# Kernel tuning notes

Measured on AMD Instinct MI355X. Metric: run time of the kernel, lower is better.

The kernel has to match this reference:

```python
import jax, jax.numpy as jnp
import numpy as np

IN_FEATURES = 4096
OUT_FEATURES = 2048
N_GROUPS = 16  # group size = IN_FEATURES // N_GROUPS = 256


def setup_inputs() -> dict:
    key = jax.random.key(0)
    k1, k2, k3, k4 = jax.random.split(key, 4)
    x = jax.random.normal(k1, (8, 64, IN_FEATURES), dtype=jnp.float32)
    # uint8 quantized weights, stored [out, in] as in the torch module
    qweight = jax.random.randint(k2, (OUT_FEATURES, IN_FEATURES), 0, 256).astype(jnp.uint8)
    # per-(out-channel, group) dequant scale and offset; scale ~ (max-min)/255 of rand weights
    qrange = jax.random.uniform(k3, (OUT_FEATURES, N_GROUPS), dtype=jnp.float32) * (2.0 / 255.0)
    qmin = -jax.random.uniform(k4, (OUT_FEATURES, N_GROUPS), dtype=jnp.float32)
    return {"x": x, "qweight": qweight, "qrange": qrange, "qmin": qmin}


def reference(x, qweight, qrange, qmin):
    # out[b,s,o] = sum_i x[b,s,i] * (q[o,i]*qrange[o,g(i)] + qmin[o,g(i)])
    B, S, IN = x.shape
    OUT, G = qrange.shape
    gs = IN // G
    xg = x.reshape(B, S, G, gs)                     # [B,S,G,gs]
    qg = qweight.reshape(OUT, G, gs).astype(x.dtype)  # [O,G,gs]
    # fused per-group dequant matmul: scale folded into the contraction
    out = jnp.einsum('bsgi,ogi,og->bso', xg, qg, qrange)
    # offset term: qmin[o,g] * sum_i_in_group x[b,s,i]
    out = out + jnp.einsum('bsg,og->bso', xg.sum(axis=-1), qmin)
    return out
```

## Files before the change

kernel.cpp:

```cpp
#include <hip/hip_runtime.h>
#include <hip/hip_bf16.h>


#define M_T 512
#define N_T 2048
#define K_T 4096
#define NGRP 16
#define BM 128
#define BN 128
#define BK 64
#define OUT_ELEMS (M_T * N_T)
#define W_ELEMS (N_T * K_T)
#define X_ELEMS (M_T * K_T)

typedef __attribute__((ext_vector_type(8))) short mfrag_t;
typedef __attribute__((ext_vector_type(8))) unsigned short u16x8;
typedef __attribute__((ext_vector_type(4))) float f32x4;

__device__ __forceinline__ unsigned short f2bf(float f) {
  union { __hip_bfloat16 h; unsigned short u; } c;
  c.h = __float2bfloat16(f);
  return c.u;
}

__device__ __forceinline__ float bf2f(unsigned short u) {
  union { unsigned int i; float f; } c;
  c.i = ((unsigned int)u) << 16;
  return c.f;
}

__global__ __launch_bounds__(256) void pack_kernel(
    const float* __restrict__ x, const int* __restrict__ qw,
    const float* __restrict__ qrange, const float* __restrict__ qmin,
    unsigned short* __restrict__ wsW, unsigned short* __restrict__ wsX) {
  const int bid = blockIdx.x;
  const int tid = threadIdx.x;
  if (bid < (W_ELEMS / 8) / 256) {
    const int gidx = bid * 256 + tid;
    const int o = gidx >> 9;
    const int k8 = gidx & 511;
    const int g = k8 >> 5;
    const float sc = qrange[o * NGRP + g];
    const float mn = qmin[o * NGRP + g];
    const int4* q = (const int4*)(qw + ((size_t)o << 12) + (k8 << 3));
    const int4 q0 = q[0], q1 = q[1];
    u16x8 p;
    p[0] = f2bf((float)q0.x * sc + mn); p[1] = f2bf((float)q0.y * sc + mn);
    p[2] = f2bf((float)q0.z * sc + mn); p[3] = f2bf((float)q0.w * sc + mn);
    p[4] = f2bf((float)q1.x * sc + mn); p[5] = f2bf((float)q1.y * sc + mn);
    p[6] = f2bf((float)q1.z * sc + mn); p[7] = f2bf((float)q1.w * sc + mn);
    *(u16x8*)(wsW + ((size_t)gidx << 3)) = p;
  } else {
    const int gidx = (bid - (W_ELEMS / 8) / 256) * 256 + tid;
    const float4* a = (const float4*)(x + ((size_t)gidx << 3));
    const float4 a0 = a[0], a1 = a[1];
    u16x8 p;
    p[0] = f2bf(a0.x); p[1] = f2bf(a0.y); p[2] = f2bf(a0.z); p[3] = f2bf(a0.w);
    p[4] = f2bf(a1.x); p[5] = f2bf(a1.y); p[6] = f2bf(a1.z); p[7] = f2bf(a1.w);
    *(u16x8*)(wsX + ((size_t)gidx << 3)) = p;
  }
}

template <int KSPLIT, bool XCDSWZ>
__global__ __launch_bounds__(512, 4) void dq_gemm_kernel(
    const unsigned short* __restrict__ wsX, const unsigned short* __restrict__ wsW,
    unsigned short* __restrict__ dst) {
  constexpr int KC = K_T / KSPLIT;
  constexpr int NTC = KC / BK;

  __shared__ __align__(16) unsigned short As[BM * BK];
  __shared__ __align__(16) unsigned short Bs[BN * BK];

  const int tid = threadIdx.x;
  int xt, yt, kc;
  if (XCDSWZ) {
    const int b = blockIdx.x;
    kc = b & 7;
    const int slot = b >> 3;
    xt = slot & 15;
    yt = slot >> 4;
  } else {
    const int b = blockIdx.x;
    xt = b & 15;
    yt = (b >> 4) & 3;
    kc = b >> 6;
  }
  const int n0 = xt * BN;
  const int m0 = yt * BM;
  const int kbase = kc * KC;

  const int lane = tid & 63;
  const int wv = tid >> 6;
  const int wm = (wv >> 2) * 64;
  const int wn = (wv & 3) * 32;
  const int lr = lane & 15;
  const int lq = lane >> 4;
  const int rxl = lr & 7;

  const int swzcol = (((lane & 7) ^ (lane >> 3)) << 3);
  const int r0 = wv * 16 + (lane >> 3);
  const int r1 = r0 + 8;
  const unsigned short* gA0 = wsX + (size_t)(m0 + r0) * K_T + kbase + swzcol;
  const unsigned short* gA1 = wsX + (size_t)(m0 + r1) * K_T + kbase + swzcol;
  const unsigned short* gB0 = wsW + (size_t)(n0 + r0) * K_T + kbase + swzcol;
  const unsigned short* gB1 = wsW + (size_t)(n0 + r1) * K_T + kbase + swzcol;
  unsigned short* lA0 = &As[wv * 1024];
  unsigned short* lA1 = &As[wv * 1024 + 512];
  unsigned short* lB0 = &Bs[wv * 1024];
  unsigned short* lB1 = &Bs[wv * 1024 + 512];

#define STAGE(T)                                                              \
  do {                                                                        \
    const size_t o_ = (size_t)(T) * BK;                                       \
    __builtin_amdgcn_global_load_lds(                                         \
        (const __attribute__((address_space(1))) void*)(gA0 + o_),            \
        (__attribute__((address_space(3))) void*)lA0, 16, 0, 0);              \
    __builtin_amdgcn_global_load_lds(                                         \
        (const __attribute__((address_space(1))) void*)(gA1 + o_),            \
        (__attribute__((address_space(3))) void*)lA1, 16, 0, 0);              \
    __builtin_amdgcn_global_load_lds(                                         \
        (const __attribute__((address_space(1))) void*)(gB0 + o_),            \
        (__attribute__((address_space(3))) void*)lB0, 16, 0, 0);              \
    __builtin_amdgcn_global_load_lds(                                         \
        (const __attribute__((address_space(1))) void*)(gB1 + o_),            \
        (__attribute__((address_space(3))) void*)lB1, 16, 0, 0);              \
  } while (0)

  f32x4 acc[4][2] = {};

  STAGE(0);
  for (int t = 0; t < NTC; ++t) {
    __syncthreads();

#pragma unroll
    for (int kk = 0; kk < 2; ++kk) {
      const int so = ((kk * 4 + lq) ^ rxl) << 3;
      mfrag_t af[4], bf[2];
#pragma unroll
      for (int fm = 0; fm < 4; ++fm)
        af[fm] = *(const mfrag_t*)&As[(wm + fm * 16 + lr) * BK + so];
#pragma unroll
      for (int fn = 0; fn < 2; ++fn)
        bf[fn] = *(const mfrag_t*)&Bs[(wn + fn * 16 + lr) * BK + so];
#pragma unroll
      for (int fm = 0; fm < 4; ++fm)
#pragma unroll
        for (int fn = 0; fn < 2; ++fn)
          acc[fm][fn] = __builtin_amdgcn_mfma_f32_16x16x32_bf16(af[fm], bf[fn], acc[fm][fn], 0, 0, 0);
    }

    if (t + 1 < NTC) {
      __syncthreads();
      STAGE(t + 1);
    }
  }
#undef STAGE

  unsigned short* base = dst + (size_t)kc * OUT_ELEMS;
#pragma unroll
  for (int fm = 0; fm < 4; ++fm) {
#pragma unroll
    for (int fn = 0; fn < 2; ++fn) {
      const int rr = m0 + wm + fm * 16 + lq * 4;
      const int c = n0 + wn + fn * 16 + lr;
      unsigned short* op = base + (size_t)rr * N_T + c;
      op[0 * (size_t)N_T] = f2bf(acc[fm][fn][0]);
      op[1 * (size_t)N_T] = f2bf(acc[fm][fn][1]);
      op[2 * (size_t)N_T] = f2bf(acc[fm][fn][2]);
      op[3 * (size_t)N_T] = f2bf(acc[fm][fn][3]);
    }
  }
}

template <int KSPLIT>
__global__ __launch_bounds__(256) void reduce_kernel(const unsigned short* __restrict__ ws,
                                                     float* __restrict__ out) {
  const int i8 = blockIdx.x * 256 + threadIdx.x;
  const size_t base = (size_t)i8 * 8;
  float s[8];
  {
    const u16x8 v = *(const u16x8*)(ws + base);
#pragma unroll
    for (int j = 0; j < 8; ++j) s[j] = bf2f(v[j]);
  }
#pragma unroll
  for (int sl = 1; sl < KSPLIT; ++sl) {
    const u16x8 v = *(const u16x8*)(ws + (size_t)sl * OUT_ELEMS + base);
#pragma unroll
    for (int j = 0; j < 8; ++j) s[j] += bf2f(v[j]);
  }
  float4* o = (float4*)(out + base);
  o[0] = make_float4(s[0], s[1], s[2], s[3]);
  o[1] = make_float4(s[4], s[5], s[6], s[7]);
}

__global__ void naive_kernel(const float* __restrict__ x, const int* __restrict__ qw,
                             const float* __restrict__ qrange, const float* __restrict__ qmin,
                             float* __restrict__ out) {
  const int idx = blockIdx.x * 256 + threadIdx.x;
  if (idx >= OUT_ELEMS) return;
  const int m = idx / N_T, n = idx % N_T;
  float s = 0.f;
  for (int g = 0; g < NGRP; ++g) {
    const float sc = qrange[n * NGRP + g], mn = qmin[n * NGRP + g];
    float d = 0.f, xs = 0.f;
    for (int k = g * 256; k < (g + 1) * 256; ++k) {
      d += x[(size_t)m * K_T + k] * (float)qw[(size_t)n * K_T + k];
      xs += x[(size_t)m * K_T + k];
    }
    s += d * sc + xs * mn;
  }
  out[idx] = s;
}

extern "C" void kernel_launch(void* const* d_in, const int* in_sizes, int n_in,
                              void* d_out, int out_size, void* d_ws, size_t ws_size,
                              hipStream_t stream) {
  const float* x = (const float*)d_in[0];
  const int* qw = (const int*)d_in[1];
  const float* qr = (const float*)d_in[2];
  const float* qm = (const float*)d_in[3];
  float* out = (float*)d_out;

  constexpr int KS = 8;
  unsigned short* wsW = (unsigned short*)d_ws;
  unsigned short* wsX = wsW + W_ELEMS;
  unsigned short* partials = wsX + X_ELEMS;
  const size_t need = (size_t)W_ELEMS * 2 + (size_t)X_ELEMS * 2 +
                      (size_t)KS * OUT_ELEMS * 2;
  if (ws_size >= need) {
    const int packblk = (W_ELEMS / 8) / 256 + (X_ELEMS / 8) / 256;
    pack_kernel<<<packblk, 256, 0, stream>>>(x, qw, qr, qm, wsW, wsX);
    const int nblk = (N_T / BN) * (M_T / BM) * KS;
    dq_gemm_kernel<KS, true><<<nblk, dim3(512, 1, 1), 0, stream>>>(wsX, wsW, partials);
    reduce_kernel<KS><<<OUT_ELEMS / 8 / 256, 256, 0, stream>>>(partials, out);
  } else {
    naive_kernel<<<(OUT_ELEMS + 255) / 256, 256, 0, stream>>>(x, qw, qr, qm, out);
  }
}
```

Measured before the change: 32.27 us.

## Enlarge GEMM M-tile to 256 with 64x64 per-wave tiles

Doubles the block tile in M from 128 to 256 and reorganizes the 8 waves into a 4x2 grid of 64x64 sub-tiles, so each wave computes 16 MFMA accumulators instead of 8. Global-to-LDS staging is restructured to match, and launch bounds are relaxed to 2 blocks per CU. The goal is more reuse of each LDS fragment per MFMA and less load traffic per unit of output. In exchange, register pressure and LDS use per block go up, and the grid halves to 256 blocks, which cuts parallelism across CUs.

```diff
diff --git a/kernel.cpp b/kernel.cpp
--- a/kernel.cpp
+++ b/kernel.cpp
@@ -6,7 +6,7 @@
 #define N_T 2048
 #define K_T 4096
 #define NGRP 16
-#define BM 128
+#define BM 256
 #define BN 128
 #define BK 64
 #define OUT_ELEMS (M_T * N_T)
@@ -61,8 +61,8 @@
   }
 }
 
-template <int KSPLIT, bool XCDSWZ>
-__global__ __launch_bounds__(512, 4) void dq_gemm_kernel(
+template <int KSPLIT>
+__global__ __launch_bounds__(512, 2) void dq_gemm_kernel(
     const unsigned short* __restrict__ wsX, const unsigned short* __restrict__ wsW,
     unsigned short* __restrict__ dst) {
   constexpr int KC = K_T / KSPLIT;
@@ -72,61 +72,47 @@
   __shared__ __align__(16) unsigned short Bs[BN * BK];
 
   const int tid = threadIdx.x;
-  int xt, yt, kc;
-  if (XCDSWZ) {
-    const int b = blockIdx.x;
-    kc = b & 7;
-    const int slot = b >> 3;
-    xt = slot & 15;
-    yt = slot >> 4;
-  } else {
-    const int b = blockIdx.x;
-    xt = b & 15;
-    yt = (b >> 4) & 3;
-    kc = b >> 6;
-  }
+  const int b = blockIdx.x;
+  const int kc = b & 7;
+  const int slot = b >> 3;
+  const int xt = slot & 15;
+  const int yt = slot >> 4;
   const int n0 = xt * BN;
   const int m0 = yt * BM;
   const int kbase = kc * KC;
 
   const int lane = tid & 63;
   const int wv = tid >> 6;
-  const int wm = (wv >> 2) * 64;
-  const int wn = (wv & 3) * 32;
+
+  const int wm = (wv >> 1) * 64;
+  const int wn = (wv & 1) * 64;
   const int lr = lane & 15;
   const int lq = lane >> 4;
   const int rxl = lr & 7;
 
-  const int swzcol = (((lane & 7) ^ (lane >> 3)) << 3);
-  const int r0 = wv * 16 + (lane >> 3);
-  const int r1 = r0 + 8;
-  const unsigned short* gA0 = wsX + (size_t)(m0 + r0) * K_T + kbase + swzcol;
-  const unsigned short* gA1 = wsX + (size_t)(m0 + r1) * K_T + kbase + swzcol;
-  const unsigned short* gB0 = wsW + (size_t)(n0 + r0) * K_T + kbase + swzcol;
-  const unsigned short* gB1 = wsW + (size_t)(n0 + r1) * K_T + kbase + swzcol;
-  unsigned short* lA0 = &As[wv * 1024];
-  unsigned short* lA1 = &As[wv * 1024 + 512];
-  unsigned short* lB0 = &Bs[wv * 1024];
-  unsigned short* lB1 = &Bs[wv * 1024 + 512];
+  const int srow8 = lane >> 3;
+  const int scol = (((lane & 7) ^ srow8) << 3);
+  const unsigned short* gA = wsX + (size_t)(m0 + wv * 32 + srow8) * K_T + kbase + scol;
+  const unsigned short* gB = wsW + (size_t)(n0 + wv * 16 + srow8) * K_T + kbase + scol;
+  unsigned short* lA = &As[wv * 32 * BK];
+  unsigned short* lB = &Bs[wv * 16 * BK];
 
 #define STAGE(T)                                                              \
   do {                                                                        \
     const size_t o_ = (size_t)(T) * BK;                                       \
-    __builtin_amdgcn_global_load_lds(                                         \
-        (const __attribute__((address_space(1))) void*)(gA0 + o_),            \
-        (__attribute__((address_space(3))) void*)lA0, 16, 0, 0);              \
-    __builtin_amdgcn_global_load_lds(                                         \
-        (const __attribute__((address_space(1))) void*)(gA1 + o_),            \
-        (__attribute__((address_space(3))) void*)lA1, 16, 0, 0);              \
-    __builtin_amdgcn_global_load_lds(                                         \
-        (const __attribute__((address_space(1))) void*)(gB0 + o_),            \
-        (__attribute__((address_space(3))) void*)lB0, 16, 0, 0);              \
-    __builtin_amdgcn_global_load_lds(                                         \
-        (const __attribute__((address_space(1))) void*)(gB1 + o_),            \
-        (__attribute__((address_space(3))) void*)lB1, 16, 0, 0);              \
+    _Pragma("unroll")                                                         \
+    for (int c_ = 0; c_ < 4; ++c_)                                            \
+      __builtin_amdgcn_global_load_lds(                                       \
+          (const __attribute__((address_space(1))) void*)(gA + o_ + (size_t)c_ * 8 * K_T), \
+          (__attribute__((address_space(3))) void*)(lA + c_ * 8 * BK), 16, 0, 0); \
+    _Pragma("unroll")                                                         \
+    for (int c_ = 0; c_ < 2; ++c_)                                            \
+      __builtin_amdgcn_global_load_lds(                                       \
+          (const __attribute__((address_space(1))) void*)(gB + o_ + (size_t)c_ * 8 * K_T), \
+          (__attribute__((address_space(3))) void*)(lB + c_ * 8 * BK), 16, 0, 0); \
   } while (0)
 
-  f32x4 acc[4][2] = {};
+  f32x4 acc[4][4] = {};
 
   STAGE(0);
   for (int t = 0; t < NTC; ++t) {
@@ -135,17 +121,17 @@
 #pragma unroll
     for (int kk = 0; kk < 2; ++kk) {
       const int so = ((kk * 4 + lq) ^ rxl) << 3;
-      mfrag_t af[4], bf[2];
+      mfrag_t af[4], bf[4];
 #pragma unroll
       for (int fm = 0; fm < 4; ++fm)
         af[fm] = *(const mfrag_t*)&As[(wm + fm * 16 + lr) * BK + so];
 #pragma unroll
-      for (int fn = 0; fn < 2; ++fn)
+      for (int fn = 0; fn < 4; ++fn)
         bf[fn] = *(const mfrag_t*)&Bs[(wn + fn * 16 + lr) * BK + so];
 #pragma unroll
       for (int fm = 0; fm < 4; ++fm)
 #pragma unroll
-        for (int fn = 0; fn < 2; ++fn)
+        for (int fn = 0; fn < 4; ++fn)
           acc[fm][fn] = __builtin_amdgcn_mfma_f32_16x16x32_bf16(af[fm], bf[fn], acc[fm][fn], 0, 0, 0);
     }
 
@@ -160,7 +146,7 @@
 #pragma unroll
   for (int fm = 0; fm < 4; ++fm) {
 #pragma unroll
-    for (int fn = 0; fn < 2; ++fn) {
+    for (int fn = 0; fn < 4; ++fn) {
       const int rr = m0 + wm + fm * 16 + lq * 4;
       const int c = n0 + wn + fn * 16 + lr;
       unsigned short* op = base + (size_t)rr * N_T + c;
@@ -232,7 +218,7 @@
     const int packblk = (W_ELEMS / 8) / 256 + (X_ELEMS / 8) / 256;
     pack_kernel<<<packblk, 256, 0, stream>>>(x, qw, qr, qm, wsW, wsX);
     const int nblk = (N_T / BN) * (M_T / BM) * KS;
-    dq_gemm_kernel<KS, true><<<nblk, dim3(512, 1, 1), 0, stream>>>(wsX, wsW, partials);
+    dq_gemm_kernel<KS><<<nblk, dim3(512, 1, 1), 0, stream>>>(wsX, wsW, partials);
     reduce_kernel<KS><<<OUT_ELEMS / 8 / 256, 256, 0, stream>>>(partials, out);
   } else {
     naive_kernel<<<(OUT_ELEMS + 255) / 256, 256, 0, stream>>>(x, qw, qr, qm, out);
```

After: 34.58 us. +7.2%, slower.

## Fuse weight dequantization into GEMM main loop, pack weights as uint8

Applied to the files above, without the earlier changes.

The pack kernel no longer dequantizes the weights to bf16. It only narrows the int32 quantized weights to a uint8 workspace. The GEMM kernel now loads the uint8 weight tile through registers, applies the per-group scale and offset, and writes bf16 into swizzled LDS, prefetching the next tile's bytes and group parameters one iteration ahead. This halves the weight workspace traffic on both write and read, at the cost of dequant ALU work and register-staged loads inside the GEMM loop instead of direct global-to-LDS copies.

```diff
diff --git a/kernel.cpp b/kernel.cpp
--- a/kernel.cpp
+++ b/kernel.cpp
@@ -31,25 +31,19 @@
 
 __global__ __launch_bounds__(256) void pack_kernel(
     const float* __restrict__ x, const int* __restrict__ qw,
-    const float* __restrict__ qrange, const float* __restrict__ qmin,
-    unsigned short* __restrict__ wsW, unsigned short* __restrict__ wsX) {
+    unsigned char* __restrict__ wsW8, unsigned short* __restrict__ wsX) {
   const int bid = blockIdx.x;
   const int tid = threadIdx.x;
   if (bid < (W_ELEMS / 8) / 256) {
     const int gidx = bid * 256 + tid;
-    const int o = gidx >> 9;
-    const int k8 = gidx & 511;
-    const int g = k8 >> 5;
-    const float sc = qrange[o * NGRP + g];
-    const float mn = qmin[o * NGRP + g];
-    const int4* q = (const int4*)(qw + ((size_t)o << 12) + (k8 << 3));
+    const int4* q = (const int4*)(qw + ((size_t)gidx << 3));
     const int4 q0 = q[0], q1 = q[1];
-    u16x8 p;
-    p[0] = f2bf((float)q0.x * sc + mn); p[1] = f2bf((float)q0.y * sc + mn);
-    p[2] = f2bf((float)q0.z * sc + mn); p[3] = f2bf((float)q0.w * sc + mn);
-    p[4] = f2bf((float)q1.x * sc + mn); p[5] = f2bf((float)q1.y * sc + mn);
-    p[6] = f2bf((float)q1.z * sc + mn); p[7] = f2bf((float)q1.w * sc + mn);
-    *(u16x8*)(wsW + ((size_t)gidx << 3)) = p;
+    unsigned int w0 = (unsigned)(q0.x & 255) | ((unsigned)(q0.y & 255) << 8) |
+                      ((unsigned)(q0.z & 255) << 16) | ((unsigned)(q0.w & 255) << 24);
+    unsigned int w1 = (unsigned)(q1.x & 255) | ((unsigned)(q1.y & 255) << 8) |
+                      ((unsigned)(q1.z & 255) << 16) | ((unsigned)(q1.w & 255) << 24);
+    uint2* o = (uint2*)(wsW8 + ((size_t)gidx << 3));
+    *o = make_uint2(w0, w1);
   } else {
     const int gidx = (bid - (W_ELEMS / 8) / 256) * 256 + tid;
     const float4* a = (const float4*)(x + ((size_t)gidx << 3));
@@ -61,9 +55,10 @@
   }
 }
 
-template <int KSPLIT, bool XCDSWZ>
+template <int KSPLIT>
 __global__ __launch_bounds__(512, 4) void dq_gemm_kernel(
-    const unsigned short* __restrict__ wsX, const unsigned short* __restrict__ wsW,
+    const unsigned short* __restrict__ wsX, const unsigned char* __restrict__ wsW8,
+    const float* __restrict__ qrange, const float* __restrict__ qmin,
     unsigned short* __restrict__ dst) {
   constexpr int KC = K_T / KSPLIT;
   constexpr int NTC = KC / BK;
@@ -72,25 +67,18 @@
   __shared__ __align__(16) unsigned short Bs[BN * BK];
 
   const int tid = threadIdx.x;
-  int xt, yt, kc;
-  if (XCDSWZ) {
-    const int b = blockIdx.x;
-    kc = b & 7;
-    const int slot = b >> 3;
-    xt = slot & 15;
-    yt = slot >> 4;
-  } else {
-    const int b = blockIdx.x;
-    xt = b & 15;
-    yt = (b >> 4) & 3;
-    kc = b >> 6;
-  }
+  const int b = blockIdx.x;
+  const int kc = b & 7;
+  const int slot = b >> 3;
+  const int xt = slot & 15;
+  const int yt = slot >> 4;
   const int n0 = xt * BN;
   const int m0 = yt * BM;
   const int kbase = kc * KC;
 
   const int lane = tid & 63;
   const int wv = tid >> 6;
+
   const int wm = (wv >> 2) * 64;
   const int wn = (wv & 3) * 32;
   const int lr = lane & 15;
@@ -102,14 +90,10 @@
   const int r1 = r0 + 8;
   const unsigned short* gA0 = wsX + (size_t)(m0 + r0) * K_T + kbase + swzcol;
   const unsigned short* gA1 = wsX + (size_t)(m0 + r1) * K_T + kbase + swzcol;
-  const unsigned short* gB0 = wsW + (size_t)(n0 + r0) * K_T + kbase + swzcol;
-  const unsigned short* gB1 = wsW + (size_t)(n0 + r1) * K_T + kbase + swzcol;
   unsigned short* lA0 = &As[wv * 1024];
   unsigned short* lA1 = &As[wv * 1024 + 512];
-  unsigned short* lB0 = &Bs[wv * 1024];
-  unsigned short* lB1 = &Bs[wv * 1024 + 512];
-
-#define STAGE(T)                                                              \
+
+#define STAGE_A(T)                                                            \
   do {                                                                        \
     const size_t o_ = (size_t)(T) * BK;                                       \
     __builtin_amdgcn_global_load_lds(                                         \
@@ -118,18 +102,50 @@
     __builtin_amdgcn_global_load_lds(                                         \
         (const __attribute__((address_space(1))) void*)(gA1 + o_),            \
         (__attribute__((address_space(3))) void*)lA1, 16, 0, 0);              \
-    __builtin_amdgcn_global_load_lds(                                         \
-        (const __attribute__((address_space(1))) void*)(gB0 + o_),            \
-        (__attribute__((address_space(3))) void*)lB0, 16, 0, 0);              \
-    __builtin_amdgcn_global_load_lds(                                         \
-        (const __attribute__((address_space(1))) void*)(gB1 + o_),            \
-        (__attribute__((address_space(3))) void*)lB1, 16, 0, 0);              \
   } while (0)
 
+  const int srow = tid >> 2;
+  const int sseg = tid & 3;
+  const unsigned char* qp8 = wsW8 + (size_t)(n0 + srow) * K_T + kbase + sseg * 16;
+  const float* qrp = qrange + (size_t)(n0 + srow) * NGRP;
+  const float* qmp = qmin + (size_t)(n0 + srow) * NGRP;
+  const int rx7 = srow & 7;
+  const int abase = srow * BK;
+  const int wslot0 = ((sseg * 2) ^ rx7) << 3;
+  const int wslot1 = ((sseg * 2 + 1) ^ rx7) << 3;
+
+  uint4 bq;
+  float sc, mn;
+  bq = *(const uint4*)(qp8);
+  sc = qrp[kc * 2];
+  mn = qmp[kc * 2];
+  STAGE_A(0);
+
   f32x4 acc[4][2] = {};
 
-  STAGE(0);
+#define DQW(W, P, J0)                                                         \
+  P[J0 + 0] = f2bf((float)((W) & 255u) * sc + mn);                            \
+  P[J0 + 1] = f2bf((float)(((W) >> 8) & 255u) * sc + mn);                     \
+  P[J0 + 2] = f2bf((float)(((W) >> 16) & 255u) * sc + mn);                    \
+  P[J0 + 3] = f2bf((float)(((W) >> 24) & 255u) * sc + mn)
+
   for (int t = 0; t < NTC; ++t) {
+    {
+      u16x8 pb0, pb1;
+      DQW(bq.x, pb0, 0);
+      DQW(bq.y, pb0, 4);
+      DQW(bq.z, pb1, 0);
+      DQW(bq.w, pb1, 4);
+      *(u16x8*)&Bs[abase + wslot0] = pb0;
+      *(u16x8*)&Bs[abase + wslot1] = pb1;
+    }
+    if (t + 1 < NTC) {
+      bq = *(const uint4*)(qp8 + (size_t)(t + 1) * BK);
+      const int g = kc * 2 + ((t + 1) >> 2);
+      sc = qrp[g];
+      mn = qmp[g];
+    }
+
     __syncthreads();
 
 #pragma unroll
@@ -151,10 +167,11 @@
 
     if (t + 1 < NTC) {
       __syncthreads();
-      STAGE(t + 1);
-    }
-  }
-#undef STAGE
+      STAGE_A(t + 1);
+    }
+  }
+#undef STAGE_A
+#undef DQW
 
   unsigned short* base = dst + (size_t)kc * OUT_ELEMS;
 #pragma unroll
@@ -223,16 +240,16 @@
   float* out = (float*)d_out;
 
   constexpr int KS = 8;
-  unsigned short* wsW = (unsigned short*)d_ws;
-  unsigned short* wsX = wsW + W_ELEMS;
+  unsigned char* wsW8 = (unsigned char*)d_ws;
+  unsigned short* wsX = (unsigned short*)(wsW8 + W_ELEMS);
   unsigned short* partials = wsX + X_ELEMS;
-  const size_t need = (size_t)W_ELEMS * 2 + (size_t)X_ELEMS * 2 +
+  const size_t need = (size_t)W_ELEMS + (size_t)X_ELEMS * 2 +
                       (size_t)KS * OUT_ELEMS * 2;
   if (ws_size >= need) {
     const int packblk = (W_ELEMS / 8) / 256 + (X_ELEMS / 8) / 256;
-    pack_kernel<<<packblk, 256, 0, stream>>>(x, qw, qr, qm, wsW, wsX);
+    pack_kernel<<<packblk, 256, 0, stream>>>(x, qw, wsW8, wsX);
     const int nblk = (N_T / BN) * (M_T / BM) * KS;
-    dq_gemm_kernel<KS, true><<<nblk, dim3(512, 1, 1), 0, stream>>>(wsX, wsW, partials);
+    dq_gemm_kernel<KS><<<nblk, dim3(512, 1, 1), 0, stream>>>(wsX, wsW8, qr, qm, partials);
     reduce_kernel<KS><<<OUT_ELEMS / 8 / 256, 256, 0, stream>>>(partials, out);
   } else {
     naive_kernel<<<(OUT_ELEMS + 255) / 256, 256, 0, stream>>>(x, qw, qr, qm, out);
```

Result: no change. 32.77 us (+1.6%).
